# Performance work log

Hardware: AMD Instinct MI355X
Metric: run time of the kernel (lower is better)

## Reference

```python
import jax, jax.numpy as jnp
import numpy as np

K = 128
HEADS = 8

def setup_inputs() -> dict:
    key = jax.random.key(0)
    ks = jax.random.split(key, 6)
    B, S = 4, 2048
    x = jax.random.normal(ks[0], (B, S, K), dtype=jnp.float32)
    sc = 1.0 / np.sqrt(K)
    Wq = jax.random.normal(ks[1], (K, K * HEADS), dtype=jnp.float32) * sc
    Wk = jax.random.normal(ks[2], (K, K * HEADS), dtype=jnp.float32) * sc
    Wv = jax.random.normal(ks[3], (K, K * HEADS), dtype=jnp.float32) * sc
    Wo = jax.random.normal(ks[4], (HEADS * K, K), dtype=jnp.float32) * (1.0 / np.sqrt(HEADS * K))
    bo = jnp.zeros((K,), dtype=jnp.float32)
    return {"x": x, "Wq": Wq, "Wk": Wk, "Wv": Wv, "Wo": Wo, "bo": bo}

def reference(x, Wq, Wk, Wv, Wo, bo):
    B, S, k = x.shape
    h = HEADS
    # projections: (B,S,k) @ (k, k*h) -> (B,S,h,k) -> (B,h,S,k)
    q = (x @ Wq).reshape(B, S, h, k).transpose(0, 2, 1, 3)
    kk = (x @ Wk).reshape(B, S, h, k).transpose(0, 2, 1, 3)
    v = (x @ Wv).reshape(B, S, h, k).transpose(0, 2, 1, 3)
    scale = k ** -0.25
    q = q * scale
    kk = kk * scale
    scores = jnp.einsum('bhqd,bhkd->bhqk', q, kk)  # (B,h,S,S)
    attn = jax.nn.softmax(scores, axis=-1)
    out = jnp.einsum('bhqk,bhkd->bhqd', attn, v)  # (B,h,S,k)
    out = out.transpose(0, 2, 1, 3).reshape(B, S, h * k)
    return out @ Wo + bo
```

## Files before the change

kernel.cpp:

```cpp
#include <hip/hip_runtime.h>


typedef __attribute__((ext_vector_type(8))) short bf16x8;
typedef __attribute__((ext_vector_type(4))) float f32x4;
typedef __attribute__((ext_vector_type(16))) float f32x16;
typedef __attribute__((ext_vector_type(4))) int i32x4;

#define LOG2E 1.4426950408889634f

__device__ __forceinline__ unsigned short f2bf(float f) {
  unsigned u = __builtin_bit_cast(unsigned, f);
  return (unsigned short)((u + 0x7fffu + ((u >> 16) & 1u)) >> 16);
}

__device__ __forceinline__ unsigned cvtpk(float lo, float hi) {
  unsigned r;
  asm("v_cvt_pk_bf16_f32 %0, %1, %2" : "=v"(r) : "v"(lo), "v"(hi));
  return r;
}

__device__ __forceinline__ float vexp2(float x) {
  float r;
  asm("v_exp_f32 %0, %1" : "=v"(r) : "v"(x));
  return r;
}

__global__ __launch_bounds__(256) void prep_kernel(const float* __restrict__ x,
    const float* __restrict__ Wq, const float* __restrict__ Wk, const float* __restrict__ Wv,
    const float* __restrict__ Wo,
    unsigned short* __restrict__ xb, unsigned short* __restrict__ Wtq,
    unsigned short* __restrict__ Wtk, unsigned short* __restrict__ Wtv,
    unsigned short* __restrict__ Wot) {
  __shared__ float tl[64][68];
  int bid = blockIdx.x, t = threadIdx.x;
  if (bid < 512) {
    int idx = (bid * 256 + t) * 8;
    f32x4 a = *(const f32x4*)(x + idx);
    f32x4 b = *(const f32x4*)(x + idx + 4);
    i32x4 o;
    o[0] = (int)cvtpk(a[0], a[1]); o[1] = (int)cvtpk(a[2], a[3]);
    o[2] = (int)cvtpk(b[0], b[1]); o[3] = (int)cvtpk(b[2], b[3]);
    *(i32x4*)(xb + idx) = o;
    return;
  }
  int tb = bid - 512;
  int which = tb >> 5, tile = tb & 31;
  const float* in; unsigned short* out; int K, N, kt_, nt_;
  if (which == 0)      { in = Wq; out = Wtq; }
  else if (which == 1) { in = Wk; out = Wtk; }
  else if (which == 2) { in = Wv; out = Wtv; }
  else                 { in = Wo; out = Wot; }
  if (which < 3) { K = 128;  N = 1024; kt_ = tile >> 4; nt_ = tile & 15; }
  else           { K = 1024; N = 128;  kt_ = tile >> 1; nt_ = tile & 1; }
  int k0 = kt_ * 64, n0 = nt_ * 64;
  int tr = t >> 4, tc = (t & 15) * 4;
#pragma unroll
  for (int i = 0; i < 4; ++i) {
    f32x4 v = *(const f32x4*)(in + (k0 + tr + i * 16) * N + n0 + tc);
#pragma unroll
    for (int j = 0; j < 4; ++j) tl[tc + j][tr + i * 16] = v[j];
  }
  __syncthreads();
  int n = t >> 2, c0 = (t & 3) * 16;
  i32x4 o1, o2;
#pragma unroll
  for (int j = 0; j < 4; ++j) o1[j] = (int)cvtpk(tl[n][c0 + 2 * j], tl[n][c0 + 2 * j + 1]);
#pragma unroll
  for (int j = 0; j < 4; ++j) o2[j] = (int)cvtpk(tl[n][c0 + 8 + 2 * j], tl[n][c0 + 9 + 2 * j]);
  *(i32x4*)(out + (n0 + n) * K + k0 + c0) = o1;
  *(i32x4*)(out + (n0 + n) * K + k0 + c0 + 8) = o2;
}

__device__ __forceinline__ void prefetch8(f32x4* r, const unsigned short* gsrc, int t) {
#pragma unroll
  for (int it = 0; it < 8; ++it) {
    int c = t + it * 256, row = c >> 4, col = c & 15;
    r[it] = *(const f32x4*)(gsrc + row * 128 + col * 8);
  }
}

__device__ __forceinline__ void write8(unsigned short* dst, const f32x4* r, int t) {
#pragma unroll
  for (int it = 0; it < 8; ++it) {
    int c = t + it * 256, row = c >> 4, col = c & 15;
    *(f32x4*)((char*)dst + row * 256 + ((col * 16) ^ ((row & 7) << 4))) = r[it];
  }
}

__device__ __forceinline__ void stage_128x128(unsigned short* dst, const unsigned short* gsrc, int t) {
#pragma unroll
  for (int it = 0; it < 8; ++it) {
    int c = t + it * 256, row = c >> 4, col = c & 15;
    *(f32x4*)((char*)dst + row * 256 + ((col * 16) ^ ((row & 7) << 4))) =
        *(const f32x4*)(gsrc + row * 128 + col * 8);
  }
}

__device__ __forceinline__ void mma128(const unsigned short* As, const unsigned short* Bs,
                                       int wm, int wn, int l, f32x4 acc[4][4]) {
  int lc = l & 15, kg = l >> 4;
#pragma unroll
  for (int kc = 0; kc < 4; ++kc) {
    bf16x8 a[4], b[4];
#pragma unroll
    for (int mi = 0; mi < 4; ++mi) {
      int ar = wm * 64 + mi * 16 + lc;
      a[mi] = *(const bf16x8*)((const char*)As + ar * 256 + ((kc * 64 + kg * 16) ^ ((ar & 7) << 4)));
    }
#pragma unroll
    for (int ni = 0; ni < 4; ++ni) {
      int br = wn * 64 + ni * 16 + lc;
      b[ni] = *(const bf16x8*)((const char*)Bs + br * 256 + ((kc * 64 + kg * 16) ^ ((br & 7) << 4)));
    }
#pragma unroll
    for (int mi = 0; mi < 4; ++mi)
#pragma unroll
      for (int ni = 0; ni < 4; ++ni)
        acc[mi][ni] = __builtin_amdgcn_mfma_f32_16x16x32_bf16(a[mi], b[ni], acc[mi][ni], 0, 0, 0);
  }
}

__global__ __launch_bounds__(256, 2) void qkv_kernel(const unsigned short* __restrict__ xb,
    const unsigned short* __restrict__ Wtq, const unsigned short* __restrict__ Wtk,
    const unsigned short* __restrict__ Wtv,
    unsigned short* __restrict__ Qb, unsigned short* __restrict__ Kb,
    unsigned short* __restrict__ Vt) {
  __shared__ unsigned short Xs[128 * 128], Ws[128 * 128];
  int m0 = blockIdx.x * 128, n0 = blockIdx.y * 128;
  int t = threadIdx.x, w = t >> 6, l = t & 63;
  int wm = w & 1, wn = w >> 1, lc = l & 15, kg = l >> 4;
  stage_128x128(Xs, xb + m0 * 128, t);
  stage_128x128(Ws, Wtq + n0 * 128, t);
  __syncthreads();

  f32x4 rw[8];
  prefetch8(rw, Wtk + n0 * 128, t);

  f32x4 acc[4][4];
#pragma unroll
  for (int mi = 0; mi < 4; ++mi)
#pragma unroll
    for (int ni = 0; ni < 4; ++ni) acc[mi][ni] = (f32x4){0.f, 0.f, 0.f, 0.f};
  mma128(Xs, Ws, wm, wn, l, acc);
  const float qscale = 0.29730177875068026f * LOG2E;
#pragma unroll
  for (int mi = 0; mi < 4; ++mi)
#pragma unroll
    for (int ni = 0; ni < 4; ++ni)
#pragma unroll
      for (int e = 0; e < 4; ++e) {
        int m = m0 + wm * 64 + mi * 16 + kg * 4 + e;
        int n = n0 + wn * 64 + ni * 16 + lc;
        int b = m >> 11, s = m & 2047, h = n >> 7, d = n & 127;
        Qb[((b * 8 + h) * 2048 + s) * 128 + d] = f2bf(acc[mi][ni][e] * qscale);
      }
  __syncthreads();
  write8(Ws, rw, t);
  __syncthreads();
  prefetch8(rw, Wtv + n0 * 128, t);

#pragma unroll
  for (int mi = 0; mi < 4; ++mi)
#pragma unroll
    for (int ni = 0; ni < 4; ++ni) acc[mi][ni] = (f32x4){0.f, 0.f, 0.f, 0.f};
  mma128(Xs, Ws, wm, wn, l, acc);
  const float kscale = 0.29730177875068026f;
#pragma unroll
  for (int mi = 0; mi < 4; ++mi)
#pragma unroll
    for (int ni = 0; ni < 4; ++ni)
#pragma unroll
      for (int e = 0; e < 4; ++e) {
        int m = m0 + wm * 64 + mi * 16 + kg * 4 + e;
        int n = n0 + wn * 64 + ni * 16 + lc;
        int b = m >> 11, s = m & 2047, h = n >> 7, d = n & 127;
        Kb[((b * 8 + h) * 2048 + s) * 128 + d] = f2bf(acc[mi][ni][e] * kscale);
      }
  __syncthreads();
  write8(Ws, rw, t);
  __syncthreads();

#pragma unroll
  for (int mi = 0; mi < 4; ++mi)
#pragma unroll
    for (int ni = 0; ni < 4; ++ni) acc[mi][ni] = (f32x4){0.f, 0.f, 0.f, 0.f};
  mma128(Ws, Xs, wm, wn, l, acc);
#pragma unroll
  for (int mi = 0; mi < 4; ++mi)
#pragma unroll
    for (int ni = 0; ni < 4; ++ni)
#pragma unroll
      for (int e = 0; e < 4; ++e) {
        int n = n0 + wm * 64 + mi * 16 + kg * 4 + e;
        int m = m0 + wn * 64 + ni * 16 + lc;
        int b = m >> 11, s = m & 2047, h = n >> 7, d = n & 127;
        Vt[((b * 8 + h) * 128 + d) * 2048 + s] = f2bf(acc[mi][ni][e]);
      }
}

__device__ __forceinline__ void qk_step(const char* Kb_, const bf16x8* qf, int lc, int hi,
                                        f32x16& s0, f32x16& s1) {
#pragma unroll
  for (int j = 0; j < 16; ++j) { s0[j] = 0.f; s1[j] = 0.f; }
  int r1 = 32 + lc;
#pragma unroll
  for (int kc = 0; kc < 8; ++kc) {
    int cb = kc * 32 + hi * 16;
    bf16x8 k0 = *(const bf16x8*)(Kb_ + lc * 256 + (cb ^ ((lc & 7) << 4)));
    bf16x8 k1 = *(const bf16x8*)(Kb_ + r1 * 256 + (cb ^ ((r1 & 7) << 4)));
    s0 = __builtin_amdgcn_mfma_f32_32x32x16_bf16(k0, qf[kc], s0, 0, 0, 0);
    s1 = __builtin_amdgcn_mfma_f32_32x32x16_bf16(k1, qf[kc], s1, 0, 0, 0);
  }
}

__global__ __launch_bounds__(256, 2) void attn_kernel(const unsigned short* __restrict__ Qb,
    const unsigned short* __restrict__ Kb, const unsigned short* __restrict__ Vt,
    unsigned short* __restrict__ att) {
  __shared__ unsigned short lds[2][16384];
  int bid = blockIdx.x;
  int fid = (bid & 7) * 64 + (bid >> 3);
  int bh = fid >> 4, qt = fid & 15;
  const unsigned short* Qp = Qb + bh * 2048 * 128;
  const unsigned short* Kp = Kb + bh * 2048 * 128;
  const unsigned short* Vp = Vt + bh * 128 * 2048;
  int t = threadIdx.x, w = t >> 6, l = t & 63, lc = l & 31, hi = l >> 5;
  int q0 = qt * 128 + w * 32;

  bf16x8 qf[8];
  {
    const unsigned short* qr_ = Qp + (q0 + lc) * 128 + hi * 8;
#pragma unroll
    for (int kc = 0; kc < 8; ++kc) qf[kc] = *(const bf16x8*)(qr_ + kc * 16);
  }

  int kcol = l & 15, vc = l & 7;
  int krow[4], vrow[4];
#pragma unroll
  for (int i = 0; i < 4; ++i) { krow[i] = w * 16 + i * 4 + (l >> 4); vrow[i] = w * 32 + i * 8 + (l >> 3); }

  f32x16 acc[4];
#pragma unroll
  for (int i = 0; i < 4; ++i)
#pragma unroll
    for (int j = 0; j < 16; ++j) acc[i][j] = 0.f;
  float m_run = -1e30f, l_run = 0.f;

  f32x4 sk[4], sv[4];
#pragma unroll
  for (int i = 0; i < 4; ++i) {
    sk[i] = *(const f32x4*)(Kp + krow[i] * 128 + kcol * 8);
    sv[i] = *(const f32x4*)(Vp + vrow[i] * 2048 + vc * 8);
  }
#pragma unroll
  for (int i = 0; i < 4; ++i) {
    *(f32x4*)((char*)&lds[0][0] + krow[i] * 256 + ((kcol * 16) ^ ((krow[i] & 7) << 4))) = sk[i];
    *(f32x4*)((char*)&lds[0][8192] + vrow[i] * 128 + ((vc * 16) ^ ((vrow[i] & 7) << 4))) = sv[i];
  }
#pragma unroll
  for (int i = 0; i < 4; ++i) {
    sk[i] = *(const f32x4*)(Kp + (64 + krow[i]) * 128 + kcol * 8);
    sv[i] = *(const f32x4*)(Vp + vrow[i] * 2048 + 64 + vc * 8);
  }
  __syncthreads();
  f32x16 s0, s1;
  qk_step((const char*)&lds[0][0], qf, lc, hi, s0, s1);

  for (int kt = 0; kt < 32; ++kt) {
    int nb = (kt + 1) & 1;

    float t8[8];
#pragma unroll
    for (int j = 0; j < 8; ++j)
      t8[j] = fmaxf(fmaxf(s0[j], s0[j + 8]), fmaxf(s1[j], s1[j + 8]));
    float pmax = fmaxf(fmaxf(fmaxf(t8[0], t8[1]), fmaxf(t8[2], t8[3])),
                       fmaxf(fmaxf(t8[4], t8[5]), fmaxf(t8[6], t8[7])));
    pmax = fmaxf(pmax, __shfl_xor(pmax, 32));
    float mold = m_run;
    bool defer = (__all(pmax <= m_run + 11.5416f) != 0);
    if (!defer) m_run = fmaxf(m_run, pmax);
#pragma unroll
    for (int j = 0; j < 16; ++j) s0[j] = vexp2(s0[j] - m_run);
#pragma unroll
    for (int j = 0; j < 16; ++j) s1[j] = vexp2(s1[j] - m_run);
    float q8[8];
#pragma unroll
    for (int j = 0; j < 8; ++j)
      q8[j] = (s0[j] + s0[j + 8]) + (s1[j] + s1[j + 8]);
    float rs = ((q8[0] + q8[1]) + (q8[2] + q8[3])) + ((q8[4] + q8[5]) + (q8[6] + q8[7]));
    rs += __shfl_xor(rs, 32);
    if (!defer) {
      float resc = vexp2(mold - m_run);
      l_run = l_run * resc + rs;
#pragma unroll
      for (int r = 0; r < 16; ++r) {
        int qr = (r & 3) + 8 * (r >> 2) + 4 * hi;
        float f = __shfl(resc, qr, 32);
#pragma unroll
        for (int dt = 0; dt < 4; ++dt) acc[dt][r] *= f;
      }
    } else {
      l_run += rs;
    }

    bf16x8 pa[4];
#define PACK(ks, SX, o) { \
      unsigned x1 = cvtpk(SX[o], SX[(o) + 1]); \
      unsigned y1 = cvtpk(SX[(o) + 4], SX[(o) + 5]); \
      unsigned x2 = cvtpk(SX[(o) + 2], SX[(o) + 3]); \
      unsigned y2 = cvtpk(SX[(o) + 6], SX[(o) + 7]); \
      asm("v_permlane32_swap_b32 %0, %1" : "+v"(x1), "+v"(y1)); \
      asm("v_permlane32_swap_b32 %0, %1" : "+v"(x2), "+v"(y2)); \
      i32x4 pp; \
      pp[0] = (int)x1; pp[1] = (int)x2; pp[2] = (int)y1; pp[3] = (int)y2; \
      pa[ks] = __builtin_bit_cast(bf16x8, pp); }
    PACK(0, s0, 0) PACK(1, s0, 8) PACK(2, s1, 0) PACK(3, s1, 8)
#undef PACK

    __syncthreads();
    if (kt < 31) {
      char* Kn = (char*)&lds[nb][0];
      char* Vn = (char*)&lds[nb][8192];
#pragma unroll
      for (int i = 0; i < 4; ++i) {
        *(f32x4*)(Kn + krow[i] * 256 + ((kcol * 16) ^ ((krow[i] & 7) << 4))) = sk[i];
        *(f32x4*)(Vn + vrow[i] * 128 + ((vc * 16) ^ ((vrow[i] & 7) << 4))) = sv[i];
      }
      if (kt < 30) {
        int kv0 = (kt + 2) * 64;
#pragma unroll
        for (int i = 0; i < 4; ++i) {
          sk[i] = *(const f32x4*)(Kp + (kv0 + krow[i]) * 128 + kcol * 8);
          sv[i] = *(const f32x4*)(Vp + vrow[i] * 2048 + kv0 + vc * 8);
        }
      }
    }
    __syncthreads();

    __builtin_amdgcn_s_setprio(1);
    if (kt < 31) qk_step((const char*)&lds[nb][0], qf, lc, hi, s0, s1);
    const char* Vb_ = (const char*)&lds[kt & 1][8192];
#pragma unroll
    for (int ks = 0; ks < 4; ++ks) {
      int cb = ks * 32 + hi * 16;
#pragma unroll
      for (int dt = 0; dt < 4; ++dt) {
        int vr = dt * 32 + lc;
        bf16x8 vb = *(const bf16x8*)(Vb_ + vr * 128 + (cb ^ ((vr & 7) << 4)));
        acc[dt] = __builtin_amdgcn_mfma_f32_32x32x16_bf16(pa[ks], vb, acc[dt], 0, 0, 0);
      }
    }
    __builtin_amdgcn_s_setprio(0);
  }

  int b = bh >> 3, h = bh & 7;
#pragma unroll
  for (int r = 0; r < 16; ++r) {
    int qr = (r & 3) + 8 * (r >> 2) + 4 * hi;
    float linv = 1.f / __shfl(l_run, qr, 32);
    unsigned short* orow = att + ((b * 2048 + (q0 + qr)) * 8 + h) * 128 + lc;
#pragma unroll
    for (int dt = 0; dt < 4; ++dt) orow[dt * 32] = f2bf(acc[dt][r] * linv);
  }
}

__device__ __forceinline__ void mfma_64x64(const unsigned short* As, const unsigned short* Bs,
                                           int w, int l, f32x4 acc[4]) {
  int lc = l & 15, kg = l >> 4;
#pragma unroll
  for (int kc = 0; kc < 4; ++kc) {
    int ar = w * 16 + lc;
    bf16x8 a = *(const bf16x8*)((const char*)As + ar * 256 + ((kc * 64 + kg * 16) ^ ((ar & 7) << 4)));
#pragma unroll
    for (int tt = 0; tt < 4; ++tt) {
      int br = tt * 16 + lc;
      bf16x8 b = *(const bf16x8*)((const char*)Bs + br * 256 + ((kc * 64 + kg * 16) ^ ((br & 7) << 4)));
      acc[tt] = __builtin_amdgcn_mfma_f32_16x16x32_bf16(a, b, acc[tt], 0, 0, 0);
    }
  }
}

__global__ __launch_bounds__(256) void out_proj_kernel(const unsigned short* __restrict__ att,
    const unsigned short* __restrict__ Wot, const float* __restrict__ bo,
    float* __restrict__ out) {
  __shared__ unsigned short As[64 * 128], Bs[64 * 128];
  int m0 = blockIdx.x * 64, n0 = blockIdx.y * 64;
  int t = threadIdx.x, w = t >> 6, l = t & 63, lc = l & 15, kg = l >> 4;
  f32x4 acc[4];
#pragma unroll
  for (int i = 0; i < 4; ++i) acc[i] = (f32x4){0.f, 0.f, 0.f, 0.f};
  f32x4 ra[4], rb[4];
#pragma unroll
  for (int it = 0; it < 4; ++it) {
    int c = t + it * 256, row = c >> 4, col = c & 15;
    ra[it] = *(const f32x4*)(att + (m0 + row) * 1024 + col * 8);
    rb[it] = *(const f32x4*)(Wot + (n0 + row) * 1024 + col * 8);
  }
  for (int kt = 0; kt < 8; ++kt) {
    if (kt) __syncthreads();
#pragma unroll
    for (int it = 0; it < 4; ++it) {
      int c = t + it * 256, row = c >> 4, col = c & 15;
      *(f32x4*)((char*)As + row * 256 + ((col * 16) ^ ((row & 7) << 4))) = ra[it];
      *(f32x4*)((char*)Bs + row * 256 + ((col * 16) ^ ((row & 7) << 4))) = rb[it];
    }
    __syncthreads();
    if (kt < 7) {
#pragma unroll
      for (int it = 0; it < 4; ++it) {
        int c = t + it * 256, row = c >> 4, col = c & 15;
        ra[it] = *(const f32x4*)(att + (m0 + row) * 1024 + (kt + 1) * 128 + col * 8);
        rb[it] = *(const f32x4*)(Wot + (n0 + row) * 1024 + (kt + 1) * 128 + col * 8);
      }
    }
    mfma_64x64(As, Bs, w, l, acc);
  }
#pragma unroll
  for (int tt = 0; tt < 4; ++tt)
#pragma unroll
    for (int e = 0; e < 4; ++e) {
      int m = m0 + w * 16 + kg * 4 + e;
      int n = n0 + tt * 16 + lc;
      out[m * 128 + n] = acc[tt][e] + bo[n];
    }
}

extern "C" void kernel_launch(void* const* d_in, const int* in_sizes, int n_in,
                              void* d_out, int out_size, void* d_ws, size_t ws_size,
                              hipStream_t stream) {
  const float* x  = (const float*)d_in[0];
  const float* Wq = (const float*)d_in[1];
  const float* Wk = (const float*)d_in[2];
  const float* Wv = (const float*)d_in[3];
  const float* Wo = (const float*)d_in[4];
  const float* bo = (const float*)d_in[5];
  float* out = (float*)d_out;
  char* ws = (char*)d_ws;
  unsigned short* xb  = (unsigned short*)(ws);
  unsigned short* Wtq = (unsigned short*)(ws + (2u << 20));
  unsigned short* Wtk = (unsigned short*)(ws + (2u << 20) + (256u << 10));
  unsigned short* Wtv = (unsigned short*)(ws + (2u << 20) + (512u << 10));
  unsigned short* Wot = (unsigned short*)(ws + (2u << 20) + (768u << 10));
  unsigned short* Qb  = (unsigned short*)(ws + (3u << 20));
  unsigned short* Kb  = (unsigned short*)(ws + (3u << 20) + (16u << 20));
  unsigned short* Vt  = (unsigned short*)(ws + (3u << 20) + (32u << 20));
  unsigned short* att = (unsigned short*)(ws + (3u << 20) + (48u << 20));

  hipLaunchKernelGGL(prep_kernel, dim3(640), dim3(256), 0, stream,
                     x, Wq, Wk, Wv, Wo, xb, Wtq, Wtk, Wtv, Wot);
  hipLaunchKernelGGL(qkv_kernel, dim3(64, 8), dim3(256), 0, stream,
                     xb, Wtq, Wtk, Wtv, Qb, Kb, Vt);
  hipLaunchKernelGGL(attn_kernel, dim3(512), dim3(256), 0, stream,
                     Qb, Kb, Vt, att);
  hipLaunchKernelGGL(out_proj_kernel, dim3(128, 2), dim3(256), 0, stream,
                     att, Wot, bo, out);
}
```

Baseline: 167.1 us.

## Split attention KV tiles across two wave groups and shrink QKV tiles

```diff
diff --git a/kernel.cpp b/kernel.cpp
--- a/kernel.cpp
+++ b/kernel.cpp
@@ -71,152 +71,150 @@
   *(i32x4*)(out + (n0 + n) * K + k0 + c0 + 8) = o2;
 }
 
-__device__ __forceinline__ void prefetch8(f32x4* r, const unsigned short* gsrc, int t) {
-#pragma unroll
-  for (int it = 0; it < 8; ++it) {
-    int c = t + it * 256, row = c >> 4, col = c & 15;
-    r[it] = *(const f32x4*)(gsrc + row * 128 + col * 8);
-  }
-}
-
-__device__ __forceinline__ void write8(unsigned short* dst, const f32x4* r, int t) {
-#pragma unroll
-  for (int it = 0; it < 8; ++it) {
-    int c = t + it * 256, row = c >> 4, col = c & 15;
-    *(f32x4*)((char*)dst + row * 256 + ((col * 16) ^ ((row & 7) << 4))) = r[it];
-  }
-}
-
-__device__ __forceinline__ void stage_128x128(unsigned short* dst, const unsigned short* gsrc, int t) {
-#pragma unroll
-  for (int it = 0; it < 8; ++it) {
+__device__ __forceinline__ void stage_64x128(unsigned short* dst, const unsigned short* gsrc, int t) {
+#pragma unroll
+  for (int it = 0; it < 4; ++it) {
     int c = t + it * 256, row = c >> 4, col = c & 15;
     *(f32x4*)((char*)dst + row * 256 + ((col * 16) ^ ((row & 7) << 4))) =
         *(const f32x4*)(gsrc + row * 128 + col * 8);
   }
 }
 
-__device__ __forceinline__ void mma128(const unsigned short* As, const unsigned short* Bs,
-                                       int wm, int wn, int l, f32x4 acc[4][4]) {
+__device__ __forceinline__ void prefetch4(f32x4* r, const unsigned short* gsrc, int t) {
+#pragma unroll
+  for (int it = 0; it < 4; ++it) {
+    int c = t + it * 256, row = c >> 4, col = c & 15;
+    r[it] = *(const f32x4*)(gsrc + row * 128 + col * 8);
+  }
+}
+
+__device__ __forceinline__ void write4(unsigned short* dst, const f32x4* r, int t) {
+#pragma unroll
+  for (int it = 0; it < 4; ++it) {
+    int c = t + it * 256, row = c >> 4, col = c & 15;
+    *(f32x4*)((char*)dst + row * 256 + ((col * 16) ^ ((row & 7) << 4))) = r[it];
+  }
+}
+
+template<int MI, int NI>
+__device__ __forceinline__ void mma_t(const unsigned short* As, const unsigned short* Bs,
+                                      int am0, int bn0, int l, f32x4 (&acc)[MI][NI]) {
   int lc = l & 15, kg = l >> 4;
 #pragma unroll
   for (int kc = 0; kc < 4; ++kc) {
-    bf16x8 a[4], b[4];
-#pragma unroll
-    for (int mi = 0; mi < 4; ++mi) {
-      int ar = wm * 64 + mi * 16 + lc;
+    bf16x8 a[MI], b[NI];
+#pragma unroll
+    for (int mi = 0; mi < MI; ++mi) {
+      int ar = am0 + mi * 16 + lc;
       a[mi] = *(const bf16x8*)((const char*)As + ar * 256 + ((kc * 64 + kg * 16) ^ ((ar & 7) << 4)));
     }
 #pragma unroll
-    for (int ni = 0; ni < 4; ++ni) {
-      int br = wn * 64 + ni * 16 + lc;
+    for (int ni = 0; ni < NI; ++ni) {
+      int br = bn0 + ni * 16 + lc;
       b[ni] = *(const bf16x8*)((const char*)Bs + br * 256 + ((kc * 64 + kg * 16) ^ ((br & 7) << 4)));
     }
 #pragma unroll
-    for (int mi = 0; mi < 4; ++mi)
-#pragma unroll
-      for (int ni = 0; ni < 4; ++ni)
+    for (int mi = 0; mi < MI; ++mi)
+#pragma unroll
+      for (int ni = 0; ni < NI; ++ni)
         acc[mi][ni] = __builtin_amdgcn_mfma_f32_16x16x32_bf16(a[mi], b[ni], acc[mi][ni], 0, 0, 0);
   }
 }
 
-__global__ __launch_bounds__(256, 2) void qkv_kernel(const unsigned short* __restrict__ xb,
+__global__ __launch_bounds__(256, 4) void qkv_kernel(const unsigned short* __restrict__ xb,
     const unsigned short* __restrict__ Wtq, const unsigned short* __restrict__ Wtk,
     const unsigned short* __restrict__ Wtv,
     unsigned short* __restrict__ Qb, unsigned short* __restrict__ Kb,
     unsigned short* __restrict__ Vt) {
-  __shared__ unsigned short Xs[128 * 128], Ws[128 * 128];
-  int m0 = blockIdx.x * 128, n0 = blockIdx.y * 128;
+  __shared__ unsigned short Xs[64 * 128], Ws[64 * 128];
+  int m0 = blockIdx.x * 64, n0 = blockIdx.y * 64;
   int t = threadIdx.x, w = t >> 6, l = t & 63;
   int wm = w & 1, wn = w >> 1, lc = l & 15, kg = l >> 4;
-  stage_128x128(Xs, xb + m0 * 128, t);
-  stage_128x128(Ws, Wtq + n0 * 128, t);
-  __syncthreads();
-
-  f32x4 rw[8];
-  prefetch8(rw, Wtk + n0 * 128, t);
-
-  f32x4 acc[4][4];
-#pragma unroll
-  for (int mi = 0; mi < 4; ++mi)
-#pragma unroll
-    for (int ni = 0; ni < 4; ++ni) acc[mi][ni] = (f32x4){0.f, 0.f, 0.f, 0.f};
-  mma128(Xs, Ws, wm, wn, l, acc);
+  stage_64x128(Xs, xb + m0 * 128, t);
+  stage_64x128(Ws, Wtq + n0 * 128, t);
+  __syncthreads();
+
+  f32x4 rw[4];
+  prefetch4(rw, Wtk + n0 * 128, t);
+
+  f32x4 acc[2][2];
+#pragma unroll
+  for (int mi = 0; mi < 2; ++mi)
+#pragma unroll
+    for (int ni = 0; ni < 2; ++ni) acc[mi][ni] = (f32x4){0.f, 0.f, 0.f, 0.f};
+  mma_t<2, 2>(Xs, Ws, wm * 32, wn * 32, l, acc);
   const float qscale = 0.29730177875068026f * LOG2E;
 #pragma unroll
-  for (int mi = 0; mi < 4; ++mi)
-#pragma unroll
-    for (int ni = 0; ni < 4; ++ni)
+  for (int mi = 0; mi < 2; ++mi)
+#pragma unroll
+    for (int ni = 0; ni < 2; ++ni)
 #pragma unroll
       for (int e = 0; e < 4; ++e) {
-        int m = m0 + wm * 64 + mi * 16 + kg * 4 + e;
-        int n = n0 + wn * 64 + ni * 16 + lc;
+        int m = m0 + wm * 32 + mi * 16 + kg * 4 + e;
+        int n = n0 + wn * 32 + ni * 16 + lc;
         int b = m >> 11, s = m & 2047, h = n >> 7, d = n & 127;
         Qb[((b * 8 + h) * 2048 + s) * 128 + d] = f2bf(acc[mi][ni][e] * qscale);
       }
   __syncthreads();
-  write8(Ws, rw, t);
-  __syncthreads();
-  prefetch8(rw, Wtv + n0 * 128, t);
-
-#pragma unroll
-  for (int mi = 0; mi < 4; ++mi)
-#pragma unroll
-    for (int ni = 0; ni < 4; ++ni) acc[mi][ni] = (f32x4){0.f, 0.f, 0.f, 0.f};
-  mma128(Xs, Ws, wm, wn, l, acc);
+  write4(Ws, rw, t);
+  __syncthreads();
+  prefetch4(rw, Wtv + n0 * 128, t);
+
+#pragma unroll
+  for (int mi = 0; mi < 2; ++mi)
+#pragma unroll
+    for (int ni = 0; ni < 2; ++ni) acc[mi][ni] = (f32x4){0.f, 0.f, 0.f, 0.f};
+  mma_t<2, 2>(Xs, Ws, wm * 32, wn * 32, l, acc);
   const float kscale = 0.29730177875068026f;
 #pragma unroll
-  for (int mi = 0; mi < 4; ++mi)
-#pragma unroll
-    for (int ni = 0; ni < 4; ++ni)
+  for (int mi = 0; mi < 2; ++mi)
+#pragma unroll
+    for (int ni = 0; ni < 2; ++ni)
 #pragma unroll
       for (int e = 0; e < 4; ++e) {
-        int m = m0 + wm * 64 + mi * 16 + kg * 4 + e;
-        int n = n0 + wn * 64 + ni * 16 + lc;
+        int m = m0 + wm * 32 + mi * 16 + kg * 4 + e;
+        int n = n0 + wn * 32 + ni * 16 + lc;
         int b = m >> 11, s = m & 2047, h = n >> 7, d = n & 127;
         Kb[((b * 8 + h) * 2048 + s) * 128 + d] = f2bf(acc[mi][ni][e] * kscale);
       }
   __syncthreads();
-  write8(Ws, rw, t);
-  __syncthreads();
-
-#pragma unroll
-  for (int mi = 0; mi < 4; ++mi)
-#pragma unroll
-    for (int ni = 0; ni < 4; ++ni) acc[mi][ni] = (f32x4){0.f, 0.f, 0.f, 0.f};
-  mma128(Ws, Xs, wm, wn, l, acc);
-#pragma unroll
-  for (int mi = 0; mi < 4; ++mi)
-#pragma unroll
-    for (int ni = 0; ni < 4; ++ni)
+  write4(Ws, rw, t);
+  __syncthreads();
+
+#pragma unroll
+  for (int mi = 0; mi < 2; ++mi)
+#pragma unroll
+    for (int ni = 0; ni < 2; ++ni) acc[mi][ni] = (f32x4){0.f, 0.f, 0.f, 0.f};
+  mma_t<2, 2>(Ws, Xs, wm * 32, wn * 32, l, acc);
+#pragma unroll
+  for (int mi = 0; mi < 2; ++mi)
+#pragma unroll
+    for (int ni = 0; ni < 2; ++ni)
 #pragma unroll
       for (int e = 0; e < 4; ++e) {
-        int n = n0 + wm * 64 + mi * 16 + kg * 4 + e;
-        int m = m0 + wn * 64 + ni * 16 + lc;
+        int n = n0 + wm * 32 + mi * 16 + kg * 4 + e;
+        int m = m0 + wn * 32 + ni * 16 + lc;
         int b = m >> 11, s = m & 2047, h = n >> 7, d = n & 127;
         Vt[((b * 8 + h) * 128 + d) * 2048 + s] = f2bf(acc[mi][ni][e]);
       }
 }
 
-__device__ __forceinline__ void qk_step(const char* Kb_, const bf16x8* qf, int lc, int hi,
-                                        f32x16& s0, f32x16& s1) {
-#pragma unroll
-  for (int j = 0; j < 16; ++j) { s0[j] = 0.f; s1[j] = 0.f; }
-  int r1 = 32 + lc;
+__device__ __forceinline__ void qk_step8(const char* Kb_, const bf16x8* qf, int kr, int hi,
+                                         f32x16& s0) {
+#pragma unroll
+  for (int j = 0; j < 16; ++j) s0[j] = 0.f;
 #pragma unroll
   for (int kc = 0; kc < 8; ++kc) {
     int cb = kc * 32 + hi * 16;
-    bf16x8 k0 = *(const bf16x8*)(Kb_ + lc * 256 + (cb ^ ((lc & 7) << 4)));
-    bf16x8 k1 = *(const bf16x8*)(Kb_ + r1 * 256 + (cb ^ ((r1 & 7) << 4)));
+    bf16x8 k0 = *(const bf16x8*)(Kb_ + kr * 256 + (cb ^ ((kr & 7) << 4)));
     s0 = __builtin_amdgcn_mfma_f32_32x32x16_bf16(k0, qf[kc], s0, 0, 0, 0);
-    s1 = __builtin_amdgcn_mfma_f32_32x32x16_bf16(k1, qf[kc], s1, 0, 0, 0);
-  }
-}
-
-__global__ __launch_bounds__(256, 2) void attn_kernel(const unsigned short* __restrict__ Qb,
+  }
+}
+
+__global__ __launch_bounds__(512, 4) void attn_kernel(const unsigned short* __restrict__ Qb,
     const unsigned short* __restrict__ Kb, const unsigned short* __restrict__ Vt,
     unsigned short* __restrict__ att) {
-  __shared__ unsigned short lds[2][16384];
+  __shared__ __align__(16) char smem[67584];
   int bid = blockIdx.x;
   int fid = (bid & 7) * 64 + (bid >> 3);
   int bh = fid >> 4, qt = fid & 15;
@@ -224,7 +222,9 @@
   const unsigned short* Kp = Kb + bh * 2048 * 128;
   const unsigned short* Vp = Vt + bh * 128 * 2048;
   int t = threadIdx.x, w = t >> 6, l = t & 63, lc = l & 31, hi = l >> 5;
-  int q0 = qt * 128 + w * 32;
+  int g = w >> 2, wl = w & 3;
+  int q0 = qt * 128 + wl * 32;
+  int kr = g * 32 + lc;
 
   bf16x8 qf[8];
   {
@@ -234,9 +234,9 @@
   }
 
   int kcol = l & 15, vc = l & 7;
-  int krow[4], vrow[4];
-#pragma unroll
-  for (int i = 0; i < 4; ++i) { krow[i] = w * 16 + i * 4 + (l >> 4); vrow[i] = w * 32 + i * 8 + (l >> 3); }
+  int krow[2], vrow[2];
+#pragma unroll
+  for (int i = 0; i < 2; ++i) { krow[i] = w * 8 + i * 4 + (l >> 4); vrow[i] = w * 16 + i * 8 + (l >> 3); }
 
   f32x16 acc[4];
 #pragma unroll
@@ -245,48 +245,45 @@
     for (int j = 0; j < 16; ++j) acc[i][j] = 0.f;
   float m_run = -1e30f, l_run = 0.f;
 
-  f32x4 sk[4], sv[4];
-#pragma unroll
-  for (int i = 0; i < 4; ++i) {
+  f32x4 sk[2], sv[2];
+#pragma unroll
+  for (int i = 0; i < 2; ++i) {
     sk[i] = *(const f32x4*)(Kp + krow[i] * 128 + kcol * 8);
     sv[i] = *(const f32x4*)(Vp + vrow[i] * 2048 + vc * 8);
   }
 #pragma unroll
-  for (int i = 0; i < 4; ++i) {
-    *(f32x4*)((char*)&lds[0][0] + krow[i] * 256 + ((kcol * 16) ^ ((krow[i] & 7) << 4))) = sk[i];
-    *(f32x4*)((char*)&lds[0][8192] + vrow[i] * 128 + ((vc * 16) ^ ((vrow[i] & 7) << 4))) = sv[i];
-  }
-#pragma unroll
-  for (int i = 0; i < 4; ++i) {
+  for (int i = 0; i < 2; ++i) {
+    *(f32x4*)(smem + krow[i] * 256 + ((kcol * 16) ^ ((krow[i] & 7) << 4))) = sk[i];
+    *(f32x4*)(smem + 16384 + vrow[i] * 128 + ((vc * 16) ^ ((vrow[i] & 7) << 4))) = sv[i];
+  }
+#pragma unroll
+  for (int i = 0; i < 2; ++i) {
     sk[i] = *(const f32x4*)(Kp + (64 + krow[i]) * 128 + kcol * 8);
     sv[i] = *(const f32x4*)(Vp + vrow[i] * 2048 + 64 + vc * 8);
   }
   __syncthreads();
-  f32x16 s0, s1;
-  qk_step((const char*)&lds[0][0], qf, lc, hi, s0, s1);
+  f32x16 s0;
+  qk_step8(smem, qf, kr, hi, s0);
 
   for (int kt = 0; kt < 32; ++kt) {
     int nb = (kt + 1) & 1;
 
-    float t8[8];
-#pragma unroll
-    for (int j = 0; j < 8; ++j)
-      t8[j] = fmaxf(fmaxf(s0[j], s0[j + 8]), fmaxf(s1[j], s1[j + 8]));
-    float pmax = fmaxf(fmaxf(fmaxf(t8[0], t8[1]), fmaxf(t8[2], t8[3])),
-                       fmaxf(fmaxf(t8[4], t8[5]), fmaxf(t8[6], t8[7])));
+    float t4[4];
+#pragma unroll
+    for (int j = 0; j < 4; ++j)
+      t4[j] = fmaxf(fmaxf(s0[j], s0[j + 4]), fmaxf(s0[j + 8], s0[j + 12]));
+    float pmax = fmaxf(fmaxf(t4[0], t4[1]), fmaxf(t4[2], t4[3]));
     pmax = fmaxf(pmax, __shfl_xor(pmax, 32));
     float mold = m_run;
     bool defer = (__all(pmax <= m_run + 11.5416f) != 0);
     if (!defer) m_run = fmaxf(m_run, pmax);
 #pragma unroll
     for (int j = 0; j < 16; ++j) s0[j] = vexp2(s0[j] - m_run);
-#pragma unroll
-    for (int j = 0; j < 16; ++j) s1[j] = vexp2(s1[j] - m_run);
-    float q8[8];
-#pragma unroll
-    for (int j = 0; j < 8; ++j)
-      q8[j] = (s0[j] + s0[j + 8]) + (s1[j] + s1[j + 8]);
-    float rs = ((q8[0] + q8[1]) + (q8[2] + q8[3])) + ((q8[4] + q8[5]) + (q8[6] + q8[7]));
+    float q4[4];
+#pragma unroll
+    for (int j = 0; j < 4; ++j)
+      q4[j] = (s0[j] + s0[j + 4]) + (s0[j + 8] + s0[j + 12]);
+    float rs = (q4[0] + q4[1]) + (q4[2] + q4[3]);
     rs += __shfl_xor(rs, 32);
     if (!defer) {
       float resc = vexp2(mold - m_run);
@@ -302,7 +299,7 @@
       l_run += rs;
     }
 
-    bf16x8 pa[4];
+    bf16x8 pa[2];
 #define PACK(ks, SX, o) { \
       unsigned x1 = cvtpk(SX[o], SX[(o) + 1]); \
       unsigned y1 = cvtpk(SX[(o) + 4], SX[(o) + 5]); \
@@ -313,22 +310,22 @@
       i32x4 pp; \
       pp[0] = (int)x1; pp[1] = (int)x2; pp[2] = (int)y1; pp[3] = (int)y2; \
       pa[ks] = __builtin_bit_cast(bf16x8, pp); }
-    PACK(0, s0, 0) PACK(1, s0, 8) PACK(2, s1, 0) PACK(3, s1, 8)
+    PACK(0, s0, 0) PACK(1, s0, 8)
 #undef PACK
 
     __syncthreads();
     if (kt < 31) {
-      char* Kn = (char*)&lds[nb][0];
-      char* Vn = (char*)&lds[nb][8192];
-#pragma unroll
-      for (int i = 0; i < 4; ++i) {
+      char* Kn = smem + (nb << 15);
+      char* Vn = Kn + 16384;
+#pragma unroll
+      for (int i = 0; i < 2; ++i) {
         *(f32x4*)(Kn + krow[i] * 256 + ((kcol * 16) ^ ((krow[i] & 7) << 4))) = sk[i];
         *(f32x4*)(Vn + vrow[i] * 128 + ((vc * 16) ^ ((vrow[i] & 7) << 4))) = sv[i];
       }
       if (kt < 30) {
         int kv0 = (kt + 2) * 64;
 #pragma unroll
-        for (int i = 0; i < 4; ++i) {
+        for (int i = 0; i < 2; ++i) {
           sk[i] = *(const f32x4*)(Kp + (kv0 + krow[i]) * 128 + kcol * 8);
           sv[i] = *(const f32x4*)(Vp + vrow[i] * 2048 + kv0 + vc * 8);
         }
@@ -337,11 +334,11 @@
     __syncthreads();
 
     __builtin_amdgcn_s_setprio(1);
-    if (kt < 31) qk_step((const char*)&lds[nb][0], qf, lc, hi, s0, s1);
-    const char* Vb_ = (const char*)&lds[kt & 1][8192];
-#pragma unroll
-    for (int ks = 0; ks < 4; ++ks) {
-      int cb = ks * 32 + hi * 16;
+    if (kt < 31) qk_step8(smem + (nb << 15), qf, kr, hi, s0);
+    const char* Vb_ = smem + ((kt & 1) << 15) + 16384;
+#pragma unroll
+    for (int ks = 0; ks < 2; ++ks) {
+      int cb = g * 64 + ks * 32 + hi * 16;
 #pragma unroll
       for (int dt = 0; dt < 4; ++dt) {
         int vr = dt * 32 + lc;
@@ -352,14 +349,39 @@
     __builtin_amdgcn_s_setprio(0);
   }
 
-  int b = bh >> 3, h = bh & 7;
-#pragma unroll
-  for (int r = 0; r < 16; ++r) {
-    int qr = (r & 3) + 8 * (r >> 2) + 4 * hi;
-    float linv = 1.f / __shfl(l_run, qr, 32);
-    unsigned short* orow = att + ((b * 2048 + (q0 + qr)) * 8 + h) * 128 + lc;
-#pragma unroll
-    for (int dt = 0; dt < 4; ++dt) orow[dt * 32] = f2bf(acc[dt][r] * linv);
+  __syncthreads();
+  float* sO = (float*)smem;
+  float* sm = (float*)(smem + 65536);
+  float* sl = (float*)(smem + 66560);
+  if (g == 1) {
+    int base = wl * 4096 + l;
+#pragma unroll
+    for (int dt = 0; dt < 4; ++dt)
+#pragma unroll
+      for (int r = 0; r < 16; ++r)
+        sO[base + dt * 1024 + r * 64] = acc[dt][r];
+    sm[wl * 64 + l] = m_run;
+    sl[wl * 64 + l] = l_run;
+  }
+  __syncthreads();
+  if (g == 0) {
+    float m1 = sm[wl * 64 + l], l1 = sl[wl * 64 + l];
+    float M = fmaxf(m_run, m1);
+    float w0 = vexp2(m_run - M), w1 = vexp2(m1 - M);
+    float lsum = l_run * w0 + l1 * w1;
+    int b = bh >> 3, h = bh & 7;
+    int base = wl * 4096 + l;
+#pragma unroll
+    for (int r = 0; r < 16; ++r) {
+      int qr = (r & 3) + 8 * (r >> 2) + 4 * hi;
+      float f0 = __shfl(w0, qr, 32);
+      float f1 = __shfl(w1, qr, 32);
+      float li = 1.f / __shfl(lsum, qr, 32);
+      unsigned short* orow = att + ((b * 2048 + (q0 + qr)) * 8 + h) * 128 + lc;
+#pragma unroll
+      for (int dt = 0; dt < 4; ++dt)
+        orow[dt * 32] = f2bf((acc[dt][r] * f0 + sO[base + dt * 1024 + r * 64] * f1) * li);
+    }
   }
 }
 
@@ -447,9 +469,9 @@
 
   hipLaunchKernelGGL(prep_kernel, dim3(640), dim3(256), 0, stream,
                      x, Wq, Wk, Wv, Wo, xb, Wtq, Wtk, Wtv, Wot);
-  hipLaunchKernelGGL(qkv_kernel, dim3(64, 8), dim3(256), 0, stream,
+  hipLaunchKernelGGL(qkv_kernel, dim3(128, 16), dim3(256), 0, stream,
                      xb, Wtq, Wtk, Wtv, Qb, Kb, Vt);
-  hipLaunchKernelGGL(attn_kernel, dim3(512), dim3(256), 0, stream,
+  hipLaunchKernelGGL(attn_kernel, dim3(512), dim3(512), 0, stream,
                      Qb, Kb, Vt, att);
   hipLaunchKernelGGL(out_proj_kernel, dim3(128, 2), dim3(256), 0, stream,
                      att, Wot, bo, out);
```

Result: slower. 364.6 us (+118.2%).
